# Kernel optimization log

Hardware: AMD Instinct MI355X
Metric: run time of the kernel (lower is better)

The kernel has to match this reference:

```python
import jax, jax.numpy as jnp
import numpy as np

N = 50000
E = 800000
NEG_SLOPE = 0.2
LN_EPS = 1e-5


def _layer_norm(x, g, b):
    mu = jnp.mean(x, axis=-1, keepdims=True)
    var = jnp.mean(jnp.square(x - mu), axis=-1, keepdims=True)
    return (x - mu) * jax.lax.rsqrt(var + LN_EPS) * g + b


def _gat(x, src, dst, W, a_s, a_d, bias, concat):
    # x: [N, Fin], W: [Fin, H*C], a_s/a_d: [H, C]
    H, C = a_s.shape
    h = (x @ W).reshape(N, H, C)
    # per-node attention logits (PyG GATConv style)
    als = jnp.sum(h * a_s, axis=-1)  # [N, H] from source nodes
    ald = jnp.sum(h * a_d, axis=-1)  # [N, H] from target nodes
    e = jax.nn.leaky_relu(als[src] + ald[dst], negative_slope=NEG_SLOPE)  # [E', H]
    # segment softmax over incoming edges of each target node
    m = jax.ops.segment_max(e, dst, num_segments=N)
    m = jnp.where(jnp.isfinite(m), m, 0.0)  # guard empty segments
    ex = jnp.exp(e - m[dst])
    denom = jax.ops.segment_sum(ex, dst, num_segments=N)
    alpha = ex / (denom[dst] + 1e-16)  # [E', H]
    out = jax.ops.segment_sum(h[src] * alpha[:, :, None], dst, num_segments=N)  # [N, H, C]
    out = out.reshape(N, H * C) if concat else jnp.mean(out, axis=1)
    return out + bias


def setup_inputs() -> dict:
    key = jax.random.key(0)
    ks = jax.random.split(key, 20)
    H, C = 4, 64
    d_in, d_hid, d_out = 128, H * C, 64
    g = lambda k, shape, fan: jax.random.normal(k, shape, jnp.float32) * (1.0 / np.sqrt(fan))
    return {
        "x": jax.random.normal(ks[0], (N, d_in), jnp.float32),
        "edge_index": jax.random.randint(ks[1], (2, E), 0, N, jnp.int64),
        "W1": g(ks[2], (d_in, H * C), d_in), "a1s": g(ks[3], (H, C), C), "a1d": g(ks[4], (H, C), C),
        "b1": jnp.zeros((d_hid,), jnp.float32), "ln1_g": jnp.ones((d_hid,), jnp.float32), "ln1_b": jnp.zeros((d_hid,), jnp.float32),
        "W2": g(ks[5], (d_hid, H * C), d_hid), "a2s": g(ks[6], (H, C), C), "a2d": g(ks[7], (H, C), C),
        "b2": jnp.zeros((d_hid,), jnp.float32), "ln2_g": jnp.ones((d_hid,), jnp.float32), "ln2_b": jnp.zeros((d_hid,), jnp.float32),
        "W3": g(ks[8], (d_hid, 1 * d_out), d_hid), "a3s": g(ks[9], (1, d_out), d_out), "a3d": g(ks[10], (1, d_out), d_out),
        "b3": jnp.zeros((d_out,), jnp.float32),
    }


def reference(x, edge_index, W1, a1s, a1d, b1, ln1_g, ln1_b,
              W2, a2s, a2d, b2, ln2_g, ln2_b, W3, a3s, a3d, b3):
    # add self loops (GATConv default add_self_loops=True)
    loops = jnp.arange(N, dtype=edge_index.dtype)
    src = jnp.concatenate([edge_index[0], loops])
    dst = jnp.concatenate([edge_index[1], loops])
    h = _gat(x, src, dst, W1, a1s, a1d, b1, concat=True)
    h = jax.nn.relu(_layer_norm(h, ln1_g, ln1_b))  # dropout = identity (eval)
    h = _gat(h, src, dst, W2, a2s, a2d, b2, concat=True)
    h = jax.nn.relu(_layer_norm(h, ln2_g, ln2_b))
    out = _gat(h, src, dst, W3, a3s, a3d, b3, concat=False)
    return out
```

## Files before the change

kernel.cpp:

```cpp
#include <hip/hip_runtime.h>
#include <math.h>


typedef _Float16 half8 __attribute__((ext_vector_type(8)));
typedef _Float16 half4v __attribute__((ext_vector_type(4)));
typedef _Float16 half2v __attribute__((ext_vector_type(2)));
typedef float float4v __attribute__((ext_vector_type(4)));

#define CSRW 64

__device__ inline float leaky02(float v) { return (v > 0.f) ? v : 0.2f * v; }

__device__ inline void gload_lds16(const void* g, void* l) {
  __builtin_amdgcn_global_load_lds(
      (const __attribute__((address_space(1))) unsigned int*)g,
      (__attribute__((address_space(3))) unsigned int*)l, 16, 0, 0);
}

__global__ void k_wt1(const float* __restrict__ W1, _Float16* __restrict__ Wt1) {
  int t = blockIdx.x * blockDim.x + threadIdx.x;
  if (t < 128 * 256) {
    int n = t >> 7, k = t & 127;
    Wt1[t] = (_Float16)W1[(size_t)k * 256 + n];
  }
}

__global__ __launch_bounds__(256) void k_fused1(
    const float* __restrict__ x, const _Float16* __restrict__ Wt1,
    _Float16* __restrict__ hbuf, const float* __restrict__ a_s,
    const float* __restrict__ a_d, float* __restrict__ als,
    float* __restrict__ ald, const int* __restrict__ ei, int E, int N,
    int* __restrict__ cnt, unsigned short* __restrict__ colidx,
    const float* __restrict__ W2, _Float16* __restrict__ Wt2,
    const float* __restrict__ W3, _Float16* __restrict__ Wt3, int ng1,
    int nsc) {
  int b = blockIdx.x;
  if (b < ng1) {
    const int M = N;
    int bx = b & 1, by = b >> 1;
    int row0 = by * 128, col0 = bx * 128;
    int tid = threadIdx.x;
    int w = tid >> 6, lane = tid & 63;
    int quad = lane >> 4, lr = lane & 15;
    int wm0 = (w >> 1) * 64;
    int wn0 = (w & 1) * 64;
    float4v acc[4][4] = {};
#pragma unroll
    for (int kk = 0; kk < 4; kk++) {
      half8 af[4], bf[4];
#pragma unroll
      for (int i = 0; i < 4; i++) {
        int row = row0 + wm0 + i * 16 + lr;
        float4 v0 = {0.f, 0.f, 0.f, 0.f}, v1 = v0;
        if (row < M) {
          const float* p = x + (size_t)row * 128 + kk * 32 + quad * 8;
          v0 = *(const float4*)p;
          v1 = *(const float4*)(p + 4);
        }
        af[i] = half8{(_Float16)v0.x, (_Float16)v0.y, (_Float16)v0.z,
                      (_Float16)v0.w, (_Float16)v1.x, (_Float16)v1.y,
                      (_Float16)v1.z, (_Float16)v1.w};
      }
#pragma unroll
      for (int j = 0; j < 4; j++)
        bf[j] = *(const half8*)(Wt1 + (size_t)(col0 + wn0 + j * 16 + lr) * 128 +
                                kk * 32 + quad * 8);
#pragma unroll
      for (int i = 0; i < 4; i++)
#pragma unroll
        for (int j = 0; j < 4; j++)
          acc[i][j] = __builtin_amdgcn_mfma_f32_16x16x32_f16(bf[j], af[i],
                                                             acc[i][j], 0, 0, 0);
    }
#pragma unroll
    for (int i = 0; i < 4; i++) {
      int row = row0 + wm0 + i * 16 + lr;
      if (row < M) {
#pragma unroll
        for (int j = 0; j < 4; j++) {
          half4v o = {(_Float16)acc[i][j][0], (_Float16)acc[i][j][1],
                      (_Float16)acc[i][j][2], (_Float16)acc[i][j][3]};
          *(half4v*)(hbuf + (size_t)row * 256 + col0 + wn0 + j * 16 + quad * 4) = o;
        }
      }
    }
    int hd = (col0 + wn0) >> 6;
    float4 as4[4], ad4[4];
#pragma unroll
    for (int j = 0; j < 4; j++) {
      as4[j] = *(const float4*)(a_s + hd * 64 + j * 16 + quad * 4);
      ad4[j] = *(const float4*)(a_d + hd * 64 + j * 16 + quad * 4);
    }
#pragma unroll
    for (int i = 0; i < 4; i++) {
      float ps = 0.f, pd = 0.f;
#pragma unroll
      for (int j = 0; j < 4; j++) {
        ps += acc[i][j][0] * as4[j].x + acc[i][j][1] * as4[j].y +
              acc[i][j][2] * as4[j].z + acc[i][j][3] * as4[j].w;
        pd += acc[i][j][0] * ad4[j].x + acc[i][j][1] * ad4[j].y +
              acc[i][j][2] * ad4[j].z + acc[i][j][3] * ad4[j].w;
      }
      ps += __shfl_xor(ps, 16, 64);
      ps += __shfl_xor(ps, 32, 64);
      pd += __shfl_xor(pd, 16, 64);
      pd += __shfl_xor(pd, 32, 64);
      int row = row0 + wm0 + i * 16 + lr;
      if (quad == 0 && row < M) {
        als[(size_t)row * 4 + hd] = ps;
        ald[(size_t)row * 4 + hd] = pd;
      }
    }
    return;
  }
  b -= ng1;
  if (b < nsc) {
    int ET = E + N;
    int b4 = (b * 256 + threadIdx.x) * 4;
    if (b4 >= ET) return;
    if (b4 + 3 < E) {
      int4 s4 = *(const int4*)(ei + b4);
      int4 d4 = *(const int4*)(ei + E + b4);
      int p0 = atomicAdd(&cnt[d4.x], 1);
      int p1 = atomicAdd(&cnt[d4.y], 1);
      int p2 = atomicAdd(&cnt[d4.z], 1);
      int p3 = atomicAdd(&cnt[d4.w], 1);
      if (p0 < CSRW) colidx[d4.x * CSRW + p0] = (unsigned short)s4.x;
      if (p1 < CSRW) colidx[d4.y * CSRW + p1] = (unsigned short)s4.y;
      if (p2 < CSRW) colidx[d4.z * CSRW + p2] = (unsigned short)s4.z;
      if (p3 < CSRW) colidx[d4.w * CSRW + p3] = (unsigned short)s4.w;
    } else {
#pragma unroll
      for (int q = 0; q < 4; q++) {
        int e = b4 + q;
        if (e < ET) {
          int s, d;
          if (e < E) { s = ei[e]; d = ei[E + e]; } else { s = e - E; d = e - E; }
          int pos = atomicAdd(&cnt[d], 1);
          if (pos < CSRW) colidx[d * CSRW + pos] = (unsigned short)s;
        }
      }
    }
    return;
  }
  b -= nsc;
  {
    int t = b * 256 + threadIdx.x;
    if (t < 256 * 256) {
      int n = t >> 8, k = t & 255;
      Wt2[t] = (_Float16)W2[(size_t)k * 256 + n];
      return;
    }
    t -= 256 * 256;
    if (t < 256 * 64) {
      int n = t >> 8, k = t & 255;
      Wt3[t] = (_Float16)W3[(size_t)k * 64 + n];
    }
  }
}

template <int BN, int TM, int TN, int WGN, int H>
__global__ __launch_bounds__(256) void k_gemm_mfma(
    const _Float16* __restrict__ A, const _Float16* __restrict__ Bt,
    _Float16* __restrict__ C, const float* __restrict__ a_s,
    const float* __restrict__ a_d, float* __restrict__ als,
    float* __restrict__ ald, int M, int K, int Nc) {
  __shared__ _Float16 As[128 * 64];
  __shared__ _Float16 Bs[BN * 64];
  int tid = threadIdx.x;
  int row0 = blockIdx.y * 128, col0 = blockIdx.x * BN;
  int w = tid >> 6, lane = tid & 63;
  int quad = lane >> 4, lr = lane & 15;
  int wm0 = (w / WGN) * (TM * 16);
  int wn0 = (w % WGN) * (TN * 16);
  float4v acc[TM][TN] = {};
  for (int k0 = 0; k0 < K; k0 += 64) {
#pragma unroll
    for (int t = 0; t < 4; t++) {
      int G = (w * 4 + t) * 64 + lane;
      int r = G >> 3, c = G & 7;
      int cg = c ^ (r & 7);
      if (row0 + r < M)
        gload_lds16(A + (size_t)(row0 + r) * K + k0 + cg * 8,
                    As + (w * 4 + t) * 512);
    }
#pragma unroll
    for (int t = 0; t < BN / 32; t++) {
      int G = (w * (BN / 32) + t) * 64 + lane;
      int n = G >> 3, c = G & 7;
      int cg = c ^ (n & 7);
      gload_lds16(Bt + (size_t)(col0 + n) * K + k0 + cg * 8,
                  Bs + (w * (BN / 32) + t) * 512);
    }
    __syncthreads();
#pragma unroll
    for (int kk = 0; kk < 2; kk++) {
      half8 af[TM], bf[TN];
#pragma unroll
      for (int i = 0; i < TM; i++) {
        int rl = wm0 + i * 16 + lr;
        int p = kk * 4 + quad;
        af[i] = *(half8*)&As[rl * 64 + ((p ^ (rl & 7)) * 8)];
      }
#pragma unroll
      for (int j = 0; j < TN; j++) {
        int nl = wn0 + j * 16 + lr;
        int p = kk * 4 + quad;
        bf[j] = *(half8*)&Bs[nl * 64 + ((p ^ (nl & 7)) * 8)];
      }
#pragma unroll
      for (int i = 0; i < TM; i++)
#pragma unroll
        for (int j = 0; j < TN; j++)
          acc[i][j] = __builtin_amdgcn_mfma_f32_16x16x32_f16(bf[j], af[i],
                                                             acc[i][j], 0, 0, 0);
    }
    __syncthreads();
  }
#pragma unroll
  for (int i = 0; i < TM; i++) {
    int row = row0 + wm0 + i * 16 + lr;
    if (row < M) {
#pragma unroll
      for (int j = 0; j < TN; j++) {
        half4v o = {(_Float16)acc[i][j][0], (_Float16)acc[i][j][1],
                    (_Float16)acc[i][j][2], (_Float16)acc[i][j][3]};
        *(half4v*)(C + (size_t)row * Nc + col0 + wn0 + j * 16 + quad * 4) = o;
      }
    }
  }
  int hd = (col0 + wn0) >> 6;
  float4 as4[TN], ad4[TN];
#pragma unroll
  for (int j = 0; j < TN; j++) {
    as4[j] = *(const float4*)(a_s + hd * 64 + j * 16 + quad * 4);
    ad4[j] = *(const float4*)(a_d + hd * 64 + j * 16 + quad * 4);
  }
#pragma unroll
  for (int i = 0; i < TM; i++) {
    float ps = 0.f, pd = 0.f;
#pragma unroll
    for (int j = 0; j < TN; j++) {
      ps += acc[i][j][0] * as4[j].x + acc[i][j][1] * as4[j].y +
            acc[i][j][2] * as4[j].z + acc[i][j][3] * as4[j].w;
      pd += acc[i][j][0] * ad4[j].x + acc[i][j][1] * ad4[j].y +
            acc[i][j][2] * ad4[j].z + acc[i][j][3] * ad4[j].w;
    }
    ps += __shfl_xor(ps, 16, 64);
    ps += __shfl_xor(ps, 32, 64);
    pd += __shfl_xor(pd, 16, 64);
    pd += __shfl_xor(pd, 32, 64);
    int row = row0 + wm0 + i * 16 + lr;
    if (quad == 0 && row < M) {
      als[(size_t)row * H + hd] = ps;
      ald[(size_t)row * H + hd] = pd;
    }
  }
}

__global__ void k_gather4(const _Float16* __restrict__ h,
                          const float* __restrict__ als,
                          const float* __restrict__ ald,
                          const int* __restrict__ cnt,
                          const unsigned short* __restrict__ colidx,
                          const float* __restrict__ bias,
                          const float* __restrict__ ln_g,
                          const float* __restrict__ ln_b,
                          _Float16* __restrict__ out, int N) {
  int wid = (blockIdx.x * blockDim.x + threadIdx.x) >> 6;
  int lane = threadIdx.x & 63;
  int half = lane >> 5, l = lane & 31;
  int node = wid * 2 + half;
  bool active = node < N;
  int hd = l >> 3;
  int ch = l * 8;
  float aldh = active ? ald[(size_t)node * 4 + hd] : 0.f;
  half2v acc[4] = {};
  float wsum = 0.f;
  int e0 = node * CSRW;
  int e1 = active ? e0 + min(cnt[node], CSRW) : e0;
  int e = e0;
  for (; e + 4 <= e1; e += 4) {
    int s0 = colidx[e], s1 = colidx[e + 1], s2 = colidx[e + 2],
        s3 = colidx[e + 3];
    float v0 = als[(size_t)s0 * 4 + hd], v1 = als[(size_t)s1 * 4 + hd],
          v2 = als[(size_t)s2 * 4 + hd], v3 = als[(size_t)s3 * 4 + hd];
    uint4 r0 = *(const uint4*)(h + (size_t)s0 * 256 + ch);
    uint4 r1 = *(const uint4*)(h + (size_t)s1 * 256 + ch);
    uint4 r2 = *(const uint4*)(h + (size_t)s2 * 256 + ch);
    uint4 r3 = *(const uint4*)(h + (size_t)s3 * 256 + ch);
    float w0 = __expf(fminf(leaky02(v0 + aldh), 19.f) - 8.f);
    float w1 = __expf(fminf(leaky02(v1 + aldh), 19.f) - 8.f);
    float w2 = __expf(fminf(leaky02(v2 + aldh), 19.f) - 8.f);
    float w3 = __expf(fminf(leaky02(v3 + aldh), 19.f) - 8.f);
    wsum += (w0 + w1) + (w2 + w3);
    _Float16 h0 = (_Float16)w0, h1 = (_Float16)w1, h2 = (_Float16)w2,
             h3 = (_Float16)w3;
    half2v W0 = {h0, h0}, W1 = {h1, h1}, W2 = {h2, h2}, W3 = {h3, h3};
    acc[0] += W0 * __builtin_bit_cast(half2v, r0.x) +
              W1 * __builtin_bit_cast(half2v, r1.x) +
              W2 * __builtin_bit_cast(half2v, r2.x) +
              W3 * __builtin_bit_cast(half2v, r3.x);
    acc[1] += W0 * __builtin_bit_cast(half2v, r0.y) +
              W1 * __builtin_bit_cast(half2v, r1.y) +
              W2 * __builtin_bit_cast(half2v, r2.y) +
              W3 * __builtin_bit_cast(half2v, r3.y);
    acc[2] += W0 * __builtin_bit_cast(half2v, r0.z) +
              W1 * __builtin_bit_cast(half2v, r1.z) +
              W2 * __builtin_bit_cast(half2v, r2.z) +
              W3 * __builtin_bit_cast(half2v, r3.z);
    acc[3] += W0 * __builtin_bit_cast(half2v, r0.w) +
              W1 * __builtin_bit_cast(half2v, r1.w) +
              W2 * __builtin_bit_cast(half2v, r2.w) +
              W3 * __builtin_bit_cast(half2v, r3.w);
  }
  for (; e < e1; e++) {
    int s = colidx[e];
    float v = als[(size_t)s * 4 + hd];
    uint4 r = *(const uint4*)(h + (size_t)s * 256 + ch);
    float w = __expf(fminf(leaky02(v + aldh), 19.f) - 8.f);
    wsum += w;
    _Float16 hw = (_Float16)w;
    half2v W = {hw, hw};
    acc[0] += W * __builtin_bit_cast(half2v, r.x);
    acc[1] += W * __builtin_bit_cast(half2v, r.y);
    acc[2] += W * __builtin_bit_cast(half2v, r.z);
    acc[3] += W * __builtin_bit_cast(half2v, r.w);
  }
  float invl = active ? (1.f / wsum) : 0.f;
  float4 bA = active ? *(const float4*)(bias + ch) : float4{0, 0, 0, 0};
  float4 bB = active ? *(const float4*)(bias + ch + 4) : float4{0, 0, 0, 0};
  float y[8];
  y[0] = (float)acc[0].x * invl + bA.x;
  y[1] = (float)acc[0].y * invl + bA.y;
  y[2] = (float)acc[1].x * invl + bA.z;
  y[3] = (float)acc[1].y * invl + bA.w;
  y[4] = (float)acc[2].x * invl + bB.x;
  y[5] = (float)acc[2].y * invl + bB.y;
  y[6] = (float)acc[3].x * invl + bB.z;
  y[7] = (float)acc[3].y * invl + bB.w;
  float s1 = 0.f;
#pragma unroll
  for (int k = 0; k < 8; k++) s1 += y[k];
#pragma unroll
  for (int msk = 16; msk > 0; msk >>= 1) s1 += __shfl_xor(s1, msk, 64);
  float mu = s1 * (1.0f / 256.0f);
  float s2 = 0.f;
#pragma unroll
  for (int k = 0; k < 8; k++) {
    float d = y[k] - mu;
    s2 += d * d;
  }
#pragma unroll
  for (int msk = 16; msk > 0; msk >>= 1) s2 += __shfl_xor(s2, msk, 64);
  float rstd = rsqrtf(s2 * (1.0f / 256.0f) + 1e-5f);
  if (active) {
    float4 gA = *(const float4*)(ln_g + ch), gB = *(const float4*)(ln_g + ch + 4);
    float4 eA = *(const float4*)(ln_b + ch), eB = *(const float4*)(ln_b + ch + 4);
    half8 o;
    o[0] = (_Float16)fmaxf((y[0] - mu) * rstd * gA.x + eA.x, 0.f);
    o[1] = (_Float16)fmaxf((y[1] - mu) * rstd * gA.y + eA.y, 0.f);
    o[2] = (_Float16)fmaxf((y[2] - mu) * rstd * gA.z + eA.z, 0.f);
    o[3] = (_Float16)fmaxf((y[3] - mu) * rstd * gA.w + eA.w, 0.f);
    o[4] = (_Float16)fmaxf((y[4] - mu) * rstd * gB.x + eB.x, 0.f);
    o[5] = (_Float16)fmaxf((y[5] - mu) * rstd * gB.y + eB.y, 0.f);
    o[6] = (_Float16)fmaxf((y[6] - mu) * rstd * gB.z + eB.z, 0.f);
    o[7] = (_Float16)fmaxf((y[7] - mu) * rstd * gB.w + eB.w, 0.f);
    *(half8*)(out + (size_t)node * 256 + ch) = o;
  }
}

__global__ void k_gather1(const _Float16* __restrict__ h,
                          const float* __restrict__ als,
                          const float* __restrict__ ald,
                          const int* __restrict__ cnt,
                          const unsigned short* __restrict__ colidx,
                          const float* __restrict__ bias,
                          float* __restrict__ out, int N) {
  int node = (blockIdx.x * blockDim.x + threadIdx.x) >> 6;
  int lane = threadIdx.x & 63;
  if (node >= N) return;
  int g = lane >> 3, t = lane & 7, ch = t * 8;
  float aldn = ald[node];
  float acc[8] = {};
  float wsum = 0.f;
  int e0 = node * CSRW;
  int e1 = e0 + min(cnt[node], CSRW);
  int e = e0 + g;
  for (; e + 8 < e1; e += 16) {
    int sA = colidx[e], sB = colidx[e + 8];
    float vA = als[sA], vB = als[sB];
    uint4 rA = *(const uint4*)(h + (size_t)sA * 64 + ch);
    uint4 rB = *(const uint4*)(h + (size_t)sB * 64 + ch);
    float wA = __expf(fminf(leaky02(vA + aldn), 19.f) - 8.f);
    float wB = __expf(fminf(leaky02(vB + aldn), 19.f) - 8.f);
    wsum += wA + wB;
    const half2v* pA = (const half2v*)&rA;
    const half2v* pB = (const half2v*)&rB;
#pragma unroll
    for (int k = 0; k < 4; k++) {
      half2v a2 = pA[k], b2 = pB[k];
      acc[2 * k + 0] += wA * (float)a2.x + wB * (float)b2.x;
      acc[2 * k + 1] += wA * (float)a2.y + wB * (float)b2.y;
    }
  }
  if (e < e1) {
    int s = colidx[e];
    float v = als[s];
    uint4 r = *(const uint4*)(h + (size_t)s * 64 + ch);
    float w = __expf(fminf(leaky02(v + aldn), 19.f) - 8.f);
    wsum += w;
    const half2v* p = (const half2v*)&r;
#pragma unroll
    for (int k = 0; k < 4; k++) {
      half2v a2 = p[k];
      acc[2 * k + 0] += w * (float)a2.x;
      acc[2 * k + 1] += w * (float)a2.y;
    }
  }
#pragma unroll
  for (int msk = 8; msk <= 32; msk <<= 1) {
#pragma unroll
    for (int k = 0; k < 8; k++) acc[k] += __shfl_xor(acc[k], msk, 64);
    wsum += __shfl_xor(wsum, msk, 64);
  }
  if (g == 0) {
    float invl = 1.f / wsum;
    float4 bA = *(const float4*)(bias + ch), bB = *(const float4*)(bias + ch + 4);
    float4 o0 = make_float4(acc[0] * invl + bA.x, acc[1] * invl + bA.y,
                            acc[2] * invl + bA.z, acc[3] * invl + bA.w);
    float4 o1 = make_float4(acc[4] * invl + bB.x, acc[5] * invl + bB.y,
                            acc[6] * invl + bB.z, acc[7] * invl + bB.w);
    *(float4*)(out + (size_t)node * 64 + ch) = o0;
    *(float4*)(out + (size_t)node * 64 + ch + 4) = o1;
  }
}

extern "C" void kernel_launch(void* const* d_in, const int* in_sizes, int n_in,
                              void* d_out, int out_size, void* d_ws,
                              size_t ws_size, hipStream_t stream) {
  const float* x   = (const float*)d_in[0];
  const int*   ei  = (const int*)d_in[1];
  const float* W1  = (const float*)d_in[2];
  const float* a1s = (const float*)d_in[3];
  const float* a1d = (const float*)d_in[4];
  const float* b1  = (const float*)d_in[5];
  const float* g1  = (const float*)d_in[6];
  const float* be1 = (const float*)d_in[7];
  const float* W2  = (const float*)d_in[8];
  const float* a2s = (const float*)d_in[9];
  const float* a2d = (const float*)d_in[10];
  const float* b2  = (const float*)d_in[11];
  const float* g2  = (const float*)d_in[12];
  const float* be2 = (const float*)d_in[13];
  const float* W3  = (const float*)d_in[14];
  const float* a3s = (const float*)d_in[15];
  const float* a3d = (const float*)d_in[16];
  const float* b3  = (const float*)d_in[17];
  float* out = (float*)d_out;

  const int Nn = in_sizes[0] / 128;
  const int E  = in_sizes[1] / 2;
  const int ET = E + Nn;

  char* wsb = (char*)d_ws;
  size_t off = 0;
  auto alloc = [&](size_t bytes) -> void* {
    void* p = wsb + off;
    off += (bytes + 255) & ~(size_t)255;
    return p;
  };
  _Float16* ah   = (_Float16*)alloc((size_t)Nn * 256 * 2);
  _Float16* hbuf = (_Float16*)alloc((size_t)Nn * 256 * 2);
  _Float16* Wt1  = (_Float16*)alloc(128 * 256 * 2);
  _Float16* Wt2  = (_Float16*)alloc(256 * 256 * 2);
  _Float16* Wt3  = (_Float16*)alloc(256 * 64 * 2);
  float* als = (float*)alloc((size_t)Nn * 4 * 4);
  float* ald = (float*)alloc((size_t)Nn * 4 * 4);
  int* cnt   = (int*)alloc((size_t)Nn * 4);
  unsigned short* colidx = (unsigned short*)alloc((size_t)Nn * CSRW * 2);
  (void)ws_size;

  hipMemsetAsync(cnt, 0, (size_t)Nn * 4, stream);
  k_wt1<<<(128 * 256 + 255) / 256, 256, 0, stream>>>(W1, Wt1);

  int ng1 = 2 * ((Nn + 127) / 128);
  int nsc = ((ET + 3) / 4 + 255) / 256;
  int ntr = (256 * 256 + 256 * 64 + 255) / 256;
  k_fused1<<<ng1 + nsc + ntr, 256, 0, stream>>>(
      x, Wt1, hbuf, a1s, a1d, als, ald, ei, E, Nn, cnt, colidx, W2, Wt2, W3,
      Wt3, ng1, nsc);

  int nwb4 = (Nn + 7) / 8;
  int nwb1 = (Nn + 3) / 4;
  dim3 g128(2, (Nn + 127) / 128);
  dim3 g64(1, (Nn + 127) / 128);

  k_gather4<<<nwb4, 256, 0, stream>>>(hbuf, als, ald, cnt, colidx, b1, g1, be1,
                                      ah, Nn);
  k_gemm_mfma<128, 4, 4, 2, 4><<<g128, 256, 0, stream>>>(
      ah, Wt2, hbuf, a2s, a2d, als, ald, Nn, 256, 256);
  k_gather4<<<nwb4, 256, 0, stream>>>(hbuf, als, ald, cnt, colidx, b2, g2, be2,
                                      ah, Nn);
  k_gemm_mfma<64, 2, 4, 1, 1><<<g64, 256, 0, stream>>>(
      ah, Wt3, hbuf, a3s, a3d, als, ald, Nn, 256, 64);
  k_gather1<<<nwb1, 256, 0, stream>>>(hbuf, als, ald, cnt, colidx, b3, out, Nn);
}
```

Measured before the change: 362.8 us.

## Split CSR build into slot-reservation atomics and a separate placement kernel

The edge-scatter part of the fused kernel now only performs the atomic slot reservation per destination and writes the reserved positions as packed bytes. A new kernel reads those slots and writes the source indices into the fixed-width column array. The aim is to separate the latency-bound atomic-then-dependent-store chain from the scattered stores, which shortens the atomic phase running alongside the GEMM. It costs an extra launch, a small slots buffer, and a second read of the edge index array.

```diff
diff --git a/kernel.cpp b/kernel.cpp
--- a/kernel.cpp
+++ b/kernel.cpp
@@ -30,7 +30,7 @@
     _Float16* __restrict__ hbuf, const float* __restrict__ a_s,
     const float* __restrict__ a_d, float* __restrict__ als,
     float* __restrict__ ald, const int* __restrict__ ei, int E, int N,
-    int* __restrict__ cnt, unsigned short* __restrict__ colidx,
+    int* __restrict__ cnt, unsigned int* __restrict__ slots32,
     const float* __restrict__ W2, _Float16* __restrict__ Wt2,
     const float* __restrict__ W3, _Float16* __restrict__ Wt3, int ng1,
     int nsc) {
@@ -116,31 +116,22 @@
   b -= ng1;
   if (b < nsc) {
     int ET = E + N;
-    int b4 = (b * 256 + threadIdx.x) * 4;
-    if (b4 >= ET) return;
-    if (b4 + 3 < E) {
-      int4 s4 = *(const int4*)(ei + b4);
-      int4 d4 = *(const int4*)(ei + E + b4);
-      int p0 = atomicAdd(&cnt[d4.x], 1);
-      int p1 = atomicAdd(&cnt[d4.y], 1);
-      int p2 = atomicAdd(&cnt[d4.z], 1);
-      int p3 = atomicAdd(&cnt[d4.w], 1);
-      if (p0 < CSRW) colidx[d4.x * CSRW + p0] = (unsigned short)s4.x;
-      if (p1 < CSRW) colidx[d4.y * CSRW + p1] = (unsigned short)s4.y;
-      if (p2 < CSRW) colidx[d4.z * CSRW + p2] = (unsigned short)s4.z;
-      if (p3 < CSRW) colidx[d4.w * CSRW + p3] = (unsigned short)s4.w;
-    } else {
-#pragma unroll
-      for (int q = 0; q < 4; q++) {
-        int e = b4 + q;
-        if (e < ET) {
-          int s, d;
-          if (e < E) { s = ei[e]; d = ei[E + e]; } else { s = e - E; d = e - E; }
-          int pos = atomicAdd(&cnt[d], 1);
-          if (pos < CSRW) colidx[d * CSRW + pos] = (unsigned short)s;
-        }
-      }
-    }
+    int t4 = b * 256 + threadIdx.x;
+    int e0 = t4 * 4;
+    if (e0 >= ET) return;
+    unsigned int packed = 0;
+#pragma unroll
+    for (int q = 0; q < 4; q++) {
+      int e = e0 + q;
+      unsigned int byte = 0xFFu;
+      if (e < ET) {
+        int d = (e < E) ? ei[E + e] : (e - E);
+        int pos = atomicAdd(&cnt[d], 1);
+        byte = (pos < CSRW) ? (unsigned int)pos : 0xFFu;
+      }
+      packed |= byte << (q * 8);
+    }
+    slots32[t4] = packed;
     return;
   }
   b -= nsc;
@@ -155,6 +146,39 @@
     if (t < 256 * 64) {
       int n = t >> 8, k = t & 255;
       Wt3[t] = (_Float16)W3[(size_t)k * 64 + n];
+    }
+  }
+}
+
+__global__ void k_place(const int* __restrict__ ei, int E, int N,
+                        const unsigned int* __restrict__ slots32,
+                        unsigned short* __restrict__ colidx) {
+  int ET = E + N;
+  int t4 = blockIdx.x * blockDim.x + threadIdx.x;
+  int e0 = t4 * 4;
+  if (e0 >= ET) return;
+  unsigned int packed = slots32[t4];
+  if (e0 + 3 < E) {
+    int4 s4 = *(const int4*)(ei + e0);
+    int4 d4 = *(const int4*)(ei + E + e0);
+    unsigned int p0 = packed & 0xFF, p1 = (packed >> 8) & 0xFF;
+    unsigned int p2 = (packed >> 16) & 0xFF, p3 = (packed >> 24) & 0xFF;
+    if (p0 != 0xFF) colidx[d4.x * CSRW + p0] = (unsigned short)s4.x;
+    if (p1 != 0xFF) colidx[d4.y * CSRW + p1] = (unsigned short)s4.y;
+    if (p2 != 0xFF) colidx[d4.z * CSRW + p2] = (unsigned short)s4.z;
+    if (p3 != 0xFF) colidx[d4.w * CSRW + p3] = (unsigned short)s4.w;
+  } else {
+#pragma unroll
+    for (int q = 0; q < 4; q++) {
+      int e = e0 + q;
+      if (e < ET) {
+        unsigned int p = (packed >> (q * 8)) & 0xFF;
+        if (p != 0xFF) {
+          int s, d;
+          if (e < E) { s = ei[e]; d = ei[E + e]; } else { s = e - E; d = e - E; }
+          colidx[d * CSRW + p] = (unsigned short)s;
+        }
+      }
     }
   }
 }
@@ -478,6 +502,7 @@
   float* als = (float*)alloc((size_t)Nn * 4 * 4);
   float* ald = (float*)alloc((size_t)Nn * 4 * 4);
   int* cnt   = (int*)alloc((size_t)Nn * 4);
+  unsigned int* slots32 = (unsigned int*)alloc((size_t)((ET + 3) / 4) * 4);
   unsigned short* colidx = (unsigned short*)alloc((size_t)Nn * CSRW * 2);
   (void)ws_size;
 
@@ -488,8 +513,9 @@
   int nsc = ((ET + 3) / 4 + 255) / 256;
   int ntr = (256 * 256 + 256 * 64 + 255) / 256;
   k_fused1<<<ng1 + nsc + ntr, 256, 0, stream>>>(
-      x, Wt1, hbuf, a1s, a1d, als, ald, ei, E, Nn, cnt, colidx, W2, Wt2, W3,
+      x, Wt1, hbuf, a1s, a1d, als, ald, ei, E, Nn, cnt, slots32, W2, Wt2, W3,
       Wt3, ng1, nsc);
+  k_place<<<nsc, 256, 0, stream>>>(ei, E, Nn, slots32, colidx);
 
   int nwb4 = (Nn + 7) / 8;
   int nwb1 = (Nn + 3) / 4;
```

Measured after the change: 357.2 us. Within noise of the previous version (-1.5%).
